# Optimization experiments

Hardware: AMD Instinct MI355X
Metric: run time of the kernel (lower is better)

Reference implementation:

```python
import jax, jax.numpy as jnp
import numpy as np

B, T, I, U = 256, 256, 512, 1024


def setup_inputs() -> dict:
    key = jax.random.key(0)
    k0, k1, k2, k3 = jax.random.split(key, 4)
    x = jax.random.normal(k0, (B, T, I), dtype=jnp.float32)
    kernel = jax.random.normal(k1, (I, 3 * U), dtype=jnp.float32) * 0.02
    recurrent_kernel = jax.random.normal(k2, (U, 3 * U), dtype=jnp.float32) * 0.02
    bias = jax.random.normal(k3, (2, 3 * U), dtype=jnp.float32) * 0.02
    return {"x": x, "kernel": kernel, "recurrent_kernel": recurrent_kernel, "bias": bias}


def reference(x, kernel, recurrent_kernel, bias):
    """Keras GRUCell (reset_after=True) unrolled over time, returning final state.

    z = sigmoid(x Wz + bz_i + h Uz + bz_r)
    r = sigmoid(x Wr + br_i + h Ur + br_r)
    hh = tanh(x Wh + bh_i + r * (h Uh + bh_r))
    h' = z * h + (1 - z) * hh
    """
    b, t, _ = x.shape
    units = recurrent_kernel.shape[0]
    b_in, b_rec = bias[0], bias[1]
    # Batch all input projections across timesteps (same math as per-step GEMMs).
    x_proj = jnp.einsum('bti,ig->btg', x, kernel) + b_in  # (B, T, 3U)

    def step(h, xp):
        rp = h @ recurrent_kernel + b_rec  # (B, 3U)
        xz, xr, xh = jnp.split(xp, 3, axis=-1)
        rz, rr, rh = jnp.split(rp, 3, axis=-1)
        z = jax.nn.sigmoid(xz + rz)
        r = jax.nn.sigmoid(xr + rr)
        hh = jnp.tanh(xh + r * rh)
        h_new = z * h + (1.0 - z) * hh
        return h_new, None

    h0 = jnp.zeros((b, units), dtype=x.dtype)
    h_final, _ = jax.lax.scan(step, h0, jnp.swapaxes(x_proj, 0, 1))  # scan over T
    return h_final
```

## Files before the change

kernel.cpp:

```cpp
#include <hip/hip_runtime.h>
#include <hip/hip_bf16.h>

typedef float f32x4 __attribute__((ext_vector_type(4)));
typedef __bf16 bf16x8 __attribute__((ext_vector_type(8)));
typedef unsigned int u32x2 __attribute__((ext_vector_type(2)));

__device__ __forceinline__ unsigned short f2b(float f) {
  unsigned u = __builtin_bit_cast(unsigned, f);
  unsigned r = (u + 0x7fffu + ((u >> 16) & 1u)) >> 16;
  return (unsigned short)r;
}
__device__ __forceinline__ float b2f(unsigned short s) {
  return __builtin_bit_cast(float, ((unsigned)s) << 16);
}

__global__ __launch_bounds__(256) void tconv(const float* __restrict__ in,
                                             unsigned short* __restrict__ out,
                                             int R, int C) {
  __shared__ unsigned short tile[32][33];
  const int tx = threadIdx.x & 31, ty = threadIdx.x >> 5;
  const int c0 = blockIdx.x * 32, r0 = blockIdx.y * 32;
#pragma unroll
  for (int p = 0; p < 4; ++p) {
    int r = ty + p * 8;
    tile[r][tx] = f2b(in[(size_t)(r0 + r) * C + c0 + tx]);
  }
  __syncthreads();
#pragma unroll
  for (int p = 0; p < 4; ++p) {
    int cc = ty + p * 8;
    out[(size_t)(c0 + cc) * R + r0 + tx] = tile[tx][cc];
  }
}

__global__ __launch_bounds__(256) void bprep(const float* __restrict__ bias,
                                             float* __restrict__ bc) {
  const int u = blockIdx.x * 256 + threadIdx.x;
  bc[u]        = bias[u]        + bias[3072 + u];
  bc[1024 + u] = bias[1024 + u] + bias[4096 + u];
  bc[2048 + u] = bias[2048 + u];
  bc[3072 + u] = bias[5120 + u];
}

__global__ __launch_bounds__(256) void hinit(unsigned short* __restrict__ hbf,
                                             float* __restrict__ h32,
                                             int* __restrict__ flags) {
  const int id = blockIdx.x * 256 + threadIdx.x;
  ((uint2*)hbf)[id] = make_uint2(0u, 0u);
  ((float4*)h32)[id] = make_float4(0.f, 0.f, 0.f, 0.f);
  if (id < 4096) flags[id] = 0;
}

__global__ __launch_bounds__(256) void xproj(
    const float* __restrict__ x,
    const unsigned short* __restrict__ Wt,
    unsigned short* __restrict__ xp,
    int t0)
{
  __shared__ unsigned short A_s[128 * 32];
  __shared__ unsigned short B_s[128 * 32];
  const int tid = threadIdx.x;
  const int lane = tid & 63, w = tid >> 6;
  const int n0 = blockIdx.x * 128;
  const int r0 = blockIdx.y * 128;
  const int wm = w >> 1, wn = w & 1;
  const int u16l = lane & 15, kq = lane >> 4;

  f32x4 acc[4][4];
#pragma unroll
  for (int i = 0; i < 4; ++i)
#pragma unroll
    for (int j = 0; j < 4; ++j) acc[i][j] = 0.0f;

  const int srow = tid >> 1;
  const int skh = tid & 1;
  const int arow_g = r0 + srow;
  const int a_tl = arow_g >> 8, a_b = arow_g & 255;
  const float* asrc = x + ((size_t)a_b * 256 + t0 + a_tl) * 512 + skh * 16;
  const unsigned short* bsrc = Wt + (size_t)(n0 + srow) * 512 + skh * 16;

  for (int kt = 0; kt < 16; ++kt) {
    const int k0 = kt * 32;
    float4 af0 = *(const float4*)(asrc + k0);
    float4 af1 = *(const float4*)(asrc + k0 + 4);
    float4 af2 = *(const float4*)(asrc + k0 + 8);
    float4 af3 = *(const float4*)(asrc + k0 + 12);
    uint4 bv0 = *(const uint4*)(bsrc + k0);
    uint4 bv1 = *(const uint4*)(bsrc + k0 + 8);
    union { unsigned short s[8]; uint4 v; } p0, p1;
    p0.s[0] = f2b(af0.x); p0.s[1] = f2b(af0.y); p0.s[2] = f2b(af0.z); p0.s[3] = f2b(af0.w);
    p0.s[4] = f2b(af1.x); p0.s[5] = f2b(af1.y); p0.s[6] = f2b(af1.z); p0.s[7] = f2b(af1.w);
    p1.s[0] = f2b(af2.x); p1.s[1] = f2b(af2.y); p1.s[2] = f2b(af2.z); p1.s[3] = f2b(af2.w);
    p1.s[4] = f2b(af3.x); p1.s[5] = f2b(af3.y); p1.s[6] = f2b(af3.z); p1.s[7] = f2b(af3.w);
    __syncthreads();
    *(uint4*)&A_s[srow * 32 + skh * 16]     = p0.v;
    *(uint4*)&A_s[srow * 32 + skh * 16 + 8] = p1.v;
    *(uint4*)&B_s[srow * 32 + skh * 16]     = bv0;
    *(uint4*)&B_s[srow * 32 + skh * 16 + 8] = bv1;
    __syncthreads();
    bf16x8 afr[4], bfr[4];
#pragma unroll
    for (int i = 0; i < 4; ++i)
      afr[i] = *(const bf16x8*)&A_s[(wm * 64 + i * 16 + u16l) * 32 + kq * 8];
#pragma unroll
    for (int j = 0; j < 4; ++j)
      bfr[j] = *(const bf16x8*)&B_s[(wn * 64 + j * 16 + u16l) * 32 + kq * 8];
#pragma unroll
    for (int i = 0; i < 4; ++i)
#pragma unroll
      for (int j = 0; j < 4; ++j)
        acc[i][j] = __builtin_amdgcn_mfma_f32_16x16x32_bf16(afr[i], bfr[j], acc[i][j], 0, 0, 0);
  }

#pragma unroll
  for (int i = 0; i < 4; ++i)
#pragma unroll
    for (int j = 0; j < 4; ++j)
#pragma unroll
      for (int v = 0; v < 4; ++v) {
        const int gr = r0 + wm * 64 + i * 16 + kq * 4 + v;
        const int gc = n0 + wn * 64 + j * 16 + u16l;
        const int gate = gc >> 10, cg = (gc >> 4) & 63, uu = gc & 15;
        const int tl = gr >> 8, b = gr & 255;
        xp[(size_t)tl * 786432 + ((size_t)(cg * 3 + gate) * 256 + b) * 16 + uu] = f2b(acc[i][j][v]);
      }
}

__device__ __forceinline__ f32x4 up4(u32x2 q) {
  f32x4 r;
  r[0] = b2f((unsigned short)(q[0] & 0xffffu));
  r[1] = b2f((unsigned short)(q[0] >> 16));
  r[2] = b2f((unsigned short)(q[1] & 0xffffu));
  r[3] = b2f((unsigned short)(q[1] >> 16));
  return r;
}

__global__ __launch_bounds__(256, 1) void gru_persist(
    const unsigned short* __restrict__ xp,
    const unsigned short* __restrict__ Ut,
    const float* __restrict__ biasC,
    unsigned short* __restrict__ hbf0,
    unsigned short* __restrict__ hbf1,
    float* __restrict__ h32,
    int* __restrict__ flags,
    float* __restrict__ out,
    int t0, int nsteps)
{
  extern __shared__ unsigned short Uls[];
  const int tid = threadIdx.x;
  const int lane = tid & 63, w = tid >> 6;
  const int u16l = lane & 15, kq = lane >> 4;
  const int cg = blockIdx.x & 63, rg = blockIdx.x >> 6;

  for (int f = tid; f < 6144; f += 256) {
    const int ln = f & 63, ks = (f >> 6) & 31, g = f >> 11;
    const int row = g * 1024 + (cg << 4) + (ln & 15);
    const int col = ks * 32 + (ln >> 4) * 8;
    *(uint4*)&Uls[f * 8] = *(const uint4*)(Ut + (size_t)row * 1024 + col);
  }

  const int rb  = (rg << 6) + (w << 4) + u16l;
  const int cu0 = (cg << 4) + (kq << 2);
  const int lofs = lane << 3;

  const f32x4 bz4  = *(const f32x4*)(biasC + cu0);
  const f32x4 br4  = *(const f32x4*)(biasC + 1024 + cu0);
  const f32x4 bhi4 = *(const f32x4*)(biasC + 2048 + cu0);
  const f32x4 bhr4 = *(const f32x4*)(biasC + 3072 + cu0);

  f32x4 hold = *(const f32x4*)(h32 + (size_t)rb * 1024 + cu0);

  __syncthreads();

  for (int lt = 0; lt < nsteps; ++lt) {
    const int t = t0 + lt;
    const unsigned short* hin  = (t & 1) ? hbf1 : hbf0;
    unsigned short*       hout = (t & 1) ? hbf0 : hbf1;
    const unsigned short* xpt = xp + (size_t)lt * 786432;
    const unsigned short* hp = hin + ((size_t)rb << 10) + (kq << 3);

    f32x4 hbuf[32];
#pragma unroll
    for (int ks = 0; ks < 32; ++ks)
      asm volatile("global_load_dwordx4 %0, %1, off offset:%2 sc1"
                   : "=v"(hbuf[ks]) : "v"(hp), "i"(ks * 64) : "memory");

    const unsigned short* xb = xpt + ((size_t)(cg * 3) * 256 + rb) * 16 + (kq << 2);
    u32x2 xzv, xrv, xhv;
    asm volatile("global_load_dwordx2 %0, %1, off" : "=v"(xzv) : "v"(xb) : "memory");
    asm volatile("global_load_dwordx2 %0, %1, off" : "=v"(xrv) : "v"(xb + 4096) : "memory");
    asm volatile("global_load_dwordx2 %0, %1, off" : "=v"(xhv) : "v"(xb + 8192) : "memory");

    f32x4 acc0 = {0.f, 0.f, 0.f, 0.f};
    f32x4 acc1 = {0.f, 0.f, 0.f, 0.f};
    f32x4 acc2 = {0.f, 0.f, 0.f, 0.f};

    asm volatile("s_waitcnt vmcnt(19)" ::: "memory");
    __builtin_amdgcn_sched_barrier(0);
#pragma unroll
    for (int ks = 0; ks < 16; ++ks) {
      const bf16x8 a0 = *(const bf16x8*)&Uls[ks * 512 + lofs];
      const bf16x8 a1 = *(const bf16x8*)&Uls[16384 + ks * 512 + lofs];
      const bf16x8 a2 = *(const bf16x8*)&Uls[32768 + ks * 512 + lofs];
      const bf16x8 bb = __builtin_bit_cast(bf16x8, hbuf[ks]);
      acc0 = __builtin_amdgcn_mfma_f32_16x16x32_bf16(a0, bb, acc0, 0, 0, 0);
      acc1 = __builtin_amdgcn_mfma_f32_16x16x32_bf16(a1, bb, acc1, 0, 0, 0);
      acc2 = __builtin_amdgcn_mfma_f32_16x16x32_bf16(a2, bb, acc2, 0, 0, 0);
    }
    asm volatile("s_waitcnt vmcnt(3)" ::: "memory");
    __builtin_amdgcn_sched_barrier(0);
#pragma unroll
    for (int ks = 16; ks < 32; ++ks) {
      const bf16x8 a0 = *(const bf16x8*)&Uls[ks * 512 + lofs];
      const bf16x8 a1 = *(const bf16x8*)&Uls[16384 + ks * 512 + lofs];
      const bf16x8 a2 = *(const bf16x8*)&Uls[32768 + ks * 512 + lofs];
      const bf16x8 bb = __builtin_bit_cast(bf16x8, hbuf[ks]);
      acc0 = __builtin_amdgcn_mfma_f32_16x16x32_bf16(a0, bb, acc0, 0, 0, 0);
      acc1 = __builtin_amdgcn_mfma_f32_16x16x32_bf16(a1, bb, acc1, 0, 0, 0);
      acc2 = __builtin_amdgcn_mfma_f32_16x16x32_bf16(a2, bb, acc2, 0, 0, 0);
    }
    asm volatile("s_waitcnt vmcnt(0)" ::: "memory");
    __builtin_amdgcn_sched_barrier(0);

    const f32x4 xz = up4(xzv), xr = up4(xrv), xh = up4(xhv);
    unsigned hw0 = 0, hw1 = 0;
#pragma unroll
    for (int v = 0; v < 4; ++v) {
      const float zpre = acc0[v] + xz[v] + bz4[v];
      const float rpre = acc1[v] + xr[v] + br4[v];
      const float rh   = acc2[v] + bhr4[v];
      const float z  = 1.f / (1.f + __expf(-zpre));
      const float rr = 1.f / (1.f + __expf(-rpre));
      const float hpre = xh[v] + bhi4[v] + rr * rh;
      const float e2 = __expf(2.f * hpre);
      const float hh = 1.f - 2.f / (e2 + 1.f);
      const float hnew = hh + z * (hold[v] - hh);
      hold[v] = hnew;
      const unsigned hb = (unsigned)f2b(hnew);
      if (v == 0) hw0 = hb;
      if (v == 1) hw0 |= hb << 16;
      if (v == 2) hw1 = hb;
      if (v == 3) hw1 |= hb << 16;
    }

    if (t == 255) {
      *(f32x4*)(out + (size_t)rb * 1024 + cu0) = hold;
    } else {
      u32x2 hv; hv[0] = hw0; hv[1] = hw1;
      asm volatile("global_store_dwordx2 %0, %1, off sc1"
                   :: "v"(hout + (size_t)rb * 1024 + cu0), "v"(hv) : "memory");
    }

    asm volatile("s_waitcnt vmcnt(0)" ::: "memory");
    __syncthreads();
    if (tid == 0)
      (void)__hip_atomic_fetch_add(&flags[blockIdx.x << 4], 1,
                                   __ATOMIC_RELAXED, __HIP_MEMORY_SCOPE_AGENT);
    if (w == 0) {
      const int want = t + 1;
      while (__hip_atomic_load(&flags[((rg << 6) | lane) << 4], __ATOMIC_RELAXED,
                               __HIP_MEMORY_SCOPE_AGENT) < want) {}
    }
    __syncthreads();
  }

  if (t0 + nsteps < 256)
    *(f32x4*)(h32 + (size_t)rb * 1024 + cu0) = hold;
}

extern "C" void kernel_launch(void* const* d_in, const int* in_sizes, int n_in,
                              void* d_out, int out_size, void* d_ws, size_t ws_size,
                              hipStream_t stream) {
  (void)in_sizes; (void)n_in; (void)out_size;
  const float* x    = (const float*)d_in[0];
  const float* Wk   = (const float*)d_in[1];
  const float* Rk   = (const float*)d_in[2];
  const float* bias = (const float*)d_in[3];
  float* out = (float*)d_out;

  char* ws = (char*)d_ws;
  unsigned short* Wt    = (unsigned short*)(ws + 0);
  unsigned short* Ut    = (unsigned short*)(ws + 3145728);
  float*          biasC = (float*)(ws + 9437184);
  unsigned short* hbf0  = (unsigned short*)(ws + 9453568);
  unsigned short* hbf1  = (unsigned short*)(ws + 9977856);
  float*          h32   = (float*)(ws + 10502144);
  int*            flags = (int*)(ws + 11550720);
  unsigned short* xp    = (unsigned short*)(ws + 11567104);

  const size_t fixed_end = 11567104;
  int CH = 256;
  while (CH > 1 && fixed_end + (size_t)CH * 1572864 > ws_size) CH >>= 1;

  static int attr_set = 0;
  if (!attr_set) {
    (void)hipFuncSetAttribute((const void*)gru_persist,
                              hipFuncAttributeMaxDynamicSharedMemorySize, 98304);
    attr_set = 1;
  }

  tconv<<<dim3(96, 16), 256, 0, stream>>>(Wk, Wt, 512, 3072);
  tconv<<<dim3(96, 32), 256, 0, stream>>>(Rk, Ut, 1024, 3072);
  bprep<<<4, 256, 0, stream>>>(bias, biasC);
  hinit<<<256, 256, 0, stream>>>(hbf0, h32, flags);

  const int nch = 256 / CH;
  for (int c = 0; c < nch; ++c) {
    xproj<<<dim3(24, CH * 2), 256, 0, stream>>>(x, Wt, xp, c * CH);
    gru_persist<<<256, 256, 98304, stream>>>(xp, Ut, biasC, hbf0, hbf1, h32,
                                             flags, out, c * CH, CH);
  }
}
```

Baseline: 2.383 ms.

## Fuse input projection into persistent GRU kernel, overlapping it with barrier wait

Removes the separate xproj GEMM and its bf16 xp intermediate. Instead, x is converted to bf16 once and each persistent block keeps its slice of W in shared memory. It computes the next step's input projection for its tile while waiting on the inter-block flag barrier, so the work is hidden in sync slack. It also drops chunked launches and the h32 state buffer. In exchange it needs more LDS (144KB) and adds per-step x loads and MFMAs to the critical loop, with a vmcnt(0) wait that may lengthen each step if the projection does not fit in the barrier wait.

```diff
diff --git a/kernel.cpp b/kernel.cpp
--- a/kernel.cpp
+++ b/kernel.cpp
@@ -2,8 +2,8 @@
 #include <hip/hip_bf16.h>
 
 typedef float f32x4 __attribute__((ext_vector_type(4)));
+typedef float f32x2 __attribute__((ext_vector_type(2)));
 typedef __bf16 bf16x8 __attribute__((ext_vector_type(8)));
-typedef unsigned int u32x2 __attribute__((ext_vector_type(2)));
 
 __device__ __forceinline__ unsigned short f2b(float f) {
   unsigned u = __builtin_bit_cast(unsigned, f);
@@ -43,110 +43,35 @@
 }
 
 __global__ __launch_bounds__(256) void hinit(unsigned short* __restrict__ hbf,
-                                             float* __restrict__ h32,
                                              int* __restrict__ flags) {
   const int id = blockIdx.x * 256 + threadIdx.x;
   ((uint2*)hbf)[id] = make_uint2(0u, 0u);
-  ((float4*)h32)[id] = make_float4(0.f, 0.f, 0.f, 0.f);
   if (id < 4096) flags[id] = 0;
 }
 
-__global__ __launch_bounds__(256) void xproj(
-    const float* __restrict__ x,
+__global__ __launch_bounds__(256) void xconv(const float* __restrict__ x,
+                                             unsigned short* __restrict__ xb) {
+  const size_t id = (size_t)blockIdx.x * 256 + threadIdx.x;
+  const float4 a = ((const float4*)x)[id * 2];
+  const float4 b = ((const float4*)x)[id * 2 + 1];
+  union { unsigned short s[8]; uint4 v; } p;
+  p.s[0] = f2b(a.x); p.s[1] = f2b(a.y); p.s[2] = f2b(a.z); p.s[3] = f2b(a.w);
+  p.s[4] = f2b(b.x); p.s[5] = f2b(b.y); p.s[6] = f2b(b.z); p.s[7] = f2b(b.w);
+  ((uint4*)xb)[id] = p.v;
+}
+
+__global__ __launch_bounds__(256, 1) void gru_persist(
+    const unsigned short* __restrict__ xbf,
+    const unsigned short* __restrict__ Ut,
     const unsigned short* __restrict__ Wt,
-    unsigned short* __restrict__ xp,
-    int t0)
-{
-  __shared__ unsigned short A_s[128 * 32];
-  __shared__ unsigned short B_s[128 * 32];
-  const int tid = threadIdx.x;
-  const int lane = tid & 63, w = tid >> 6;
-  const int n0 = blockIdx.x * 128;
-  const int r0 = blockIdx.y * 128;
-  const int wm = w >> 1, wn = w & 1;
-  const int u16l = lane & 15, kq = lane >> 4;
-
-  f32x4 acc[4][4];
-#pragma unroll
-  for (int i = 0; i < 4; ++i)
-#pragma unroll
-    for (int j = 0; j < 4; ++j) acc[i][j] = 0.0f;
-
-  const int srow = tid >> 1;
-  const int skh = tid & 1;
-  const int arow_g = r0 + srow;
-  const int a_tl = arow_g >> 8, a_b = arow_g & 255;
-  const float* asrc = x + ((size_t)a_b * 256 + t0 + a_tl) * 512 + skh * 16;
-  const unsigned short* bsrc = Wt + (size_t)(n0 + srow) * 512 + skh * 16;
-
-  for (int kt = 0; kt < 16; ++kt) {
-    const int k0 = kt * 32;
-    float4 af0 = *(const float4*)(asrc + k0);
-    float4 af1 = *(const float4*)(asrc + k0 + 4);
-    float4 af2 = *(const float4*)(asrc + k0 + 8);
-    float4 af3 = *(const float4*)(asrc + k0 + 12);
-    uint4 bv0 = *(const uint4*)(bsrc + k0);
-    uint4 bv1 = *(const uint4*)(bsrc + k0 + 8);
-    union { unsigned short s[8]; uint4 v; } p0, p1;
-    p0.s[0] = f2b(af0.x); p0.s[1] = f2b(af0.y); p0.s[2] = f2b(af0.z); p0.s[3] = f2b(af0.w);
-    p0.s[4] = f2b(af1.x); p0.s[5] = f2b(af1.y); p0.s[6] = f2b(af1.z); p0.s[7] = f2b(af1.w);
-    p1.s[0] = f2b(af2.x); p1.s[1] = f2b(af2.y); p1.s[2] = f2b(af2.z); p1.s[3] = f2b(af2.w);
-    p1.s[4] = f2b(af3.x); p1.s[5] = f2b(af3.y); p1.s[6] = f2b(af3.z); p1.s[7] = f2b(af3.w);
-    __syncthreads();
-    *(uint4*)&A_s[srow * 32 + skh * 16]     = p0.v;
-    *(uint4*)&A_s[srow * 32 + skh * 16 + 8] = p1.v;
-    *(uint4*)&B_s[srow * 32 + skh * 16]     = bv0;
-    *(uint4*)&B_s[srow * 32 + skh * 16 + 8] = bv1;
-    __syncthreads();
-    bf16x8 afr[4], bfr[4];
-#pragma unroll
-    for (int i = 0; i < 4; ++i)
-      afr[i] = *(const bf16x8*)&A_s[(wm * 64 + i * 16 + u16l) * 32 + kq * 8];
-#pragma unroll
-    for (int j = 0; j < 4; ++j)
-      bfr[j] = *(const bf16x8*)&B_s[(wn * 64 + j * 16 + u16l) * 32 + kq * 8];
-#pragma unroll
-    for (int i = 0; i < 4; ++i)
-#pragma unroll
-      for (int j = 0; j < 4; ++j)
-        acc[i][j] = __builtin_amdgcn_mfma_f32_16x16x32_bf16(afr[i], bfr[j], acc[i][j], 0, 0, 0);
-  }
-
-#pragma unroll
-  for (int i = 0; i < 4; ++i)
-#pragma unroll
-    for (int j = 0; j < 4; ++j)
-#pragma unroll
-      for (int v = 0; v < 4; ++v) {
-        const int gr = r0 + wm * 64 + i * 16 + kq * 4 + v;
-        const int gc = n0 + wn * 64 + j * 16 + u16l;
-        const int gate = gc >> 10, cg = (gc >> 4) & 63, uu = gc & 15;
-        const int tl = gr >> 8, b = gr & 255;
-        xp[(size_t)tl * 786432 + ((size_t)(cg * 3 + gate) * 256 + b) * 16 + uu] = f2b(acc[i][j][v]);
-      }
-}
-
-__device__ __forceinline__ f32x4 up4(u32x2 q) {
-  f32x4 r;
-  r[0] = b2f((unsigned short)(q[0] & 0xffffu));
-  r[1] = b2f((unsigned short)(q[0] >> 16));
-  r[2] = b2f((unsigned short)(q[1] & 0xffffu));
-  r[3] = b2f((unsigned short)(q[1] >> 16));
-  return r;
-}
-
-__global__ __launch_bounds__(256, 1) void gru_persist(
-    const unsigned short* __restrict__ xp,
-    const unsigned short* __restrict__ Ut,
     const float* __restrict__ biasC,
     unsigned short* __restrict__ hbf0,
     unsigned short* __restrict__ hbf1,
-    float* __restrict__ h32,
     int* __restrict__ flags,
-    float* __restrict__ out,
-    int t0, int nsteps)
+    float* __restrict__ out)
 {
   extern __shared__ unsigned short Uls[];
+  unsigned short* const Wls = Uls + 49152;
   const int tid = threadIdx.x;
   const int lane = tid & 63, w = tid >> 6;
   const int u16l = lane & 15, kq = lane >> 4;
@@ -158,6 +83,12 @@
     const int col = ks * 32 + (ln >> 4) * 8;
     *(uint4*)&Uls[f * 8] = *(const uint4*)(Ut + (size_t)row * 1024 + col);
   }
+  for (int f = tid; f < 3072; f += 256) {
+    const int ln = f & 63, ks = (f >> 6) & 15, g = f >> 10;
+    const int row = g * 1024 + (cg << 4) + (ln & 15);
+    const int col = ks * 32 + (ln >> 4) * 8;
+    *(uint4*)&Wls[f * 8] = *(const uint4*)(Wt + (size_t)row * 512 + col);
+  }
 
   const int rb  = (rg << 6) + (w << 4) + u16l;
   const int cu0 = (cg << 4) + (kq << 2);
@@ -168,15 +99,37 @@
   const f32x4 bhi4 = *(const f32x4*)(biasC + 2048 + cu0);
   const f32x4 bhr4 = *(const f32x4*)(biasC + 3072 + cu0);
 
-  f32x4 hold = *(const f32x4*)(h32 + (size_t)rb * 1024 + cu0);
+  f32x4 hold = {0.f, 0.f, 0.f, 0.f};
 
   __syncthreads();
 
-  for (int lt = 0; lt < nsteps; ++lt) {
-    const int t = t0 + lt;
+  f32x4 xzv, xrv, xhv;
+  {
+    const unsigned short* xb = xbf + ((size_t)rb * 256 + 0) * 512 + (kq << 3);
+    f32x4 xf[16];
+#pragma unroll
+    for (int ks = 0; ks < 16; ++ks)
+      asm volatile("global_load_dwordx4 %0, %1, off offset:%2"
+                   : "=v"(xf[ks]) : "v"(xb), "i"(ks * 64) : "memory");
+    asm volatile("s_waitcnt vmcnt(0)" ::: "memory");
+    __builtin_amdgcn_sched_barrier(0);
+    f32x4 a0 = {0.f,0.f,0.f,0.f}, a1 = {0.f,0.f,0.f,0.f}, a2 = {0.f,0.f,0.f,0.f};
+#pragma unroll
+    for (int ks = 0; ks < 16; ++ks) {
+      const bf16x8 w0 = *(const bf16x8*)&Wls[ks * 512 + lofs];
+      const bf16x8 w1 = *(const bf16x8*)&Wls[8192 + ks * 512 + lofs];
+      const bf16x8 w2 = *(const bf16x8*)&Wls[16384 + ks * 512 + lofs];
+      const bf16x8 bx = __builtin_bit_cast(bf16x8, xf[ks]);
+      a0 = __builtin_amdgcn_mfma_f32_16x16x32_bf16(w0, bx, a0, 0, 0, 0);
+      a1 = __builtin_amdgcn_mfma_f32_16x16x32_bf16(w1, bx, a1, 0, 0, 0);
+      a2 = __builtin_amdgcn_mfma_f32_16x16x32_bf16(w2, bx, a2, 0, 0, 0);
+    }
+    xzv = a0; xrv = a1; xhv = a2;
+  }
+
+  for (int t = 0; t < 256; ++t) {
     const unsigned short* hin  = (t & 1) ? hbf1 : hbf0;
     unsigned short*       hout = (t & 1) ? hbf0 : hbf1;
-    const unsigned short* xpt = xp + (size_t)lt * 786432;
     const unsigned short* hp = hin + ((size_t)rb << 10) + (kq << 3);
 
     f32x4 hbuf[32];
@@ -185,17 +138,11 @@
       asm volatile("global_load_dwordx4 %0, %1, off offset:%2 sc1"
                    : "=v"(hbuf[ks]) : "v"(hp), "i"(ks * 64) : "memory");
 
-    const unsigned short* xb = xpt + ((size_t)(cg * 3) * 256 + rb) * 16 + (kq << 2);
-    u32x2 xzv, xrv, xhv;
-    asm volatile("global_load_dwordx2 %0, %1, off" : "=v"(xzv) : "v"(xb) : "memory");
-    asm volatile("global_load_dwordx2 %0, %1, off" : "=v"(xrv) : "v"(xb + 4096) : "memory");
-    asm volatile("global_load_dwordx2 %0, %1, off" : "=v"(xhv) : "v"(xb + 8192) : "memory");
-
     f32x4 acc0 = {0.f, 0.f, 0.f, 0.f};
     f32x4 acc1 = {0.f, 0.f, 0.f, 0.f};
     f32x4 acc2 = {0.f, 0.f, 0.f, 0.f};
 
-    asm volatile("s_waitcnt vmcnt(19)" ::: "memory");
+    asm volatile("s_waitcnt vmcnt(16)" ::: "memory");
     __builtin_amdgcn_sched_barrier(0);
 #pragma unroll
     for (int ks = 0; ks < 16; ++ks) {
@@ -207,7 +154,7 @@
       acc1 = __builtin_amdgcn_mfma_f32_16x16x32_bf16(a1, bb, acc1, 0, 0, 0);
       acc2 = __builtin_amdgcn_mfma_f32_16x16x32_bf16(a2, bb, acc2, 0, 0, 0);
     }
-    asm volatile("s_waitcnt vmcnt(3)" ::: "memory");
+    asm volatile("s_waitcnt vmcnt(0)" ::: "memory");
     __builtin_amdgcn_sched_barrier(0);
 #pragma unroll
     for (int ks = 16; ks < 32; ++ks) {
@@ -219,19 +166,16 @@
       acc1 = __builtin_amdgcn_mfma_f32_16x16x32_bf16(a1, bb, acc1, 0, 0, 0);
       acc2 = __builtin_amdgcn_mfma_f32_16x16x32_bf16(a2, bb, acc2, 0, 0, 0);
     }
-    asm volatile("s_waitcnt vmcnt(0)" ::: "memory");
-    __builtin_amdgcn_sched_barrier(0);
-
-    const f32x4 xz = up4(xzv), xr = up4(xrv), xh = up4(xhv);
+
     unsigned hw0 = 0, hw1 = 0;
 #pragma unroll
     for (int v = 0; v < 4; ++v) {
-      const float zpre = acc0[v] + xz[v] + bz4[v];
-      const float rpre = acc1[v] + xr[v] + br4[v];
+      const float zpre = acc0[v] + xzv[v] + bz4[v];
+      const float rpre = acc1[v] + xrv[v] + br4[v];
       const float rh   = acc2[v] + bhr4[v];
       const float z  = 1.f / (1.f + __expf(-zpre));
       const float rr = 1.f / (1.f + __expf(-rpre));
-      const float hpre = xh[v] + bhi4[v] + rr * rh;
+      const float hpre = xhv[v] + bhi4[v] + rr * rh;
       const float e2 = __expf(2.f * hpre);
       const float hh = 1.f - 2.f / (e2 + 1.f);
       const float hnew = hh + z * (hold[v] - hh);
@@ -245,8 +189,13 @@
 
     if (t == 255) {
       *(f32x4*)(out + (size_t)rb * 1024 + cu0) = hold;
-    } else {
-      u32x2 hv; hv[0] = hw0; hv[1] = hw1;
+      break;
+    }
+
+    {
+      f32x2 hv;
+      hv[0] = __builtin_bit_cast(float, hw0);
+      hv[1] = __builtin_bit_cast(float, hw1);
       asm volatile("global_store_dwordx2 %0, %1, off sc1"
                    :: "v"(hout + (size_t)rb * 1024 + cu0), "v"(hv) : "memory");
     }
@@ -256,6 +205,30 @@
     if (tid == 0)
       (void)__hip_atomic_fetch_add(&flags[blockIdx.x << 4], 1,
                                    __ATOMIC_RELAXED, __HIP_MEMORY_SCOPE_AGENT);
+
+    {
+      const unsigned short* xb = xbf + ((size_t)rb * 256 + (t + 1)) * 512 + (kq << 3);
+      f32x4 xf[16];
+#pragma unroll
+      for (int ks = 0; ks < 16; ++ks)
+        asm volatile("global_load_dwordx4 %0, %1, off offset:%2"
+                     : "=v"(xf[ks]) : "v"(xb), "i"(ks * 64) : "memory");
+      asm volatile("s_waitcnt vmcnt(0)" ::: "memory");
+      __builtin_amdgcn_sched_barrier(0);
+      f32x4 a0 = {0.f,0.f,0.f,0.f}, a1 = {0.f,0.f,0.f,0.f}, a2 = {0.f,0.f,0.f,0.f};
+#pragma unroll
+      for (int ks = 0; ks < 16; ++ks) {
+        const bf16x8 w0 = *(const bf16x8*)&Wls[ks * 512 + lofs];
+        const bf16x8 w1 = *(const bf16x8*)&Wls[8192 + ks * 512 + lofs];
+        const bf16x8 w2 = *(const bf16x8*)&Wls[16384 + ks * 512 + lofs];
+        const bf16x8 bx = __builtin_bit_cast(bf16x8, xf[ks]);
+        a0 = __builtin_amdgcn_mfma_f32_16x16x32_bf16(w0, bx, a0, 0, 0, 0);
+        a1 = __builtin_amdgcn_mfma_f32_16x16x32_bf16(w1, bx, a1, 0, 0, 0);
+        a2 = __builtin_amdgcn_mfma_f32_16x16x32_bf16(w2, bx, a2, 0, 0, 0);
+      }
+      xzv = a0; xrv = a1; xhv = a2;
+    }
+
     if (w == 0) {
       const int want = t + 1;
       while (__hip_atomic_load(&flags[((rg << 6) | lane) << 4], __ATOMIC_RELAXED,
@@ -263,15 +236,12 @@
     }
     __syncthreads();
   }
-
-  if (t0 + nsteps < 256)
-    *(f32x4*)(h32 + (size_t)rb * 1024 + cu0) = hold;
 }
 
 extern "C" void kernel_launch(void* const* d_in, const int* in_sizes, int n_in,
                               void* d_out, int out_size, void* d_ws, size_t ws_size,
                               hipStream_t stream) {
-  (void)in_sizes; (void)n_in; (void)out_size;
+  (void)in_sizes; (void)n_in; (void)out_size; (void)ws_size;
   const float* x    = (const float*)d_in[0];
   const float* Wk   = (const float*)d_in[1];
   const float* Rk   = (const float*)d_in[2];
@@ -284,30 +254,22 @@
   float*          biasC = (float*)(ws + 9437184);
   unsigned short* hbf0  = (unsigned short*)(ws + 9453568);
   unsigned short* hbf1  = (unsigned short*)(ws + 9977856);
-  float*          h32   = (float*)(ws + 10502144);
-  int*            flags = (int*)(ws + 11550720);
-  unsigned short* xp    = (unsigned short*)(ws + 11567104);
-
-  const size_t fixed_end = 11567104;
-  int CH = 256;
-  while (CH > 1 && fixed_end + (size_t)CH * 1572864 > ws_size) CH >>= 1;
+  int*            flags = (int*)(ws + 10502144);
+  unsigned short* xbf   = (unsigned short*)(ws + 10518528);
 
   static int attr_set = 0;
   if (!attr_set) {
     (void)hipFuncSetAttribute((const void*)gru_persist,
-                              hipFuncAttributeMaxDynamicSharedMemorySize, 98304);
+                              hipFuncAttributeMaxDynamicSharedMemorySize, 147456);
     attr_set = 1;
   }
 
   tconv<<<dim3(96, 16), 256, 0, stream>>>(Wk, Wt, 512, 3072);
   tconv<<<dim3(96, 32), 256, 0, stream>>>(Rk, Ut, 1024, 3072);
   bprep<<<4, 256, 0, stream>>>(bias, biasC);
-  hinit<<<256, 256, 0, stream>>>(hbf0, h32, flags);
-
-  const int nch = 256 / CH;
-  for (int c = 0; c < nch; ++c) {
-    xproj<<<dim3(24, CH * 2), 256, 0, stream>>>(x, Wt, xp, c * CH);
-    gru_persist<<<256, 256, 98304, stream>>>(xp, Ut, biasC, hbf0, hbf1, h32,
-                                             flags, out, c * CH, CH);
-  }
-}
+  hinit<<<256, 256, 0, stream>>>(hbf0, flags);
+  xconv<<<16384, 256, 0, stream>>>(x, xbf);
+
+  gru_persist<<<256, 256, 147456, stream>>>(xbf, Ut, Wt, biasC,
+                                            hbf0, hbf1, flags, out);
+}
```

New measurement: 2.426 ms. Within noise of the previous version (+1.8%).
